# Kernel optimization log

Hardware: AMD Instinct MI355X
Metric: run time of the kernel (lower is better)

Reference implementation:

```python
import jax, jax.numpy as jnp
import numpy as np

N, E, D_IN, D, H, L, D_EMB, T = 4096, 131072, 72, 256, 8, 2, 128, 5
HD = D // H
LN_EPS = 1e-5


def _linear(x, w, b):
    # torch Linear: w is [out, in]
    return x @ w.T + b


def _layernorm(x, g, b):
    mu = jnp.mean(x, axis=-1, keepdims=True)
    var = jnp.var(x, axis=-1, keepdims=True)
    return (x - mu) * jax.lax.rsqrt(var + LN_EPS) * g + b


def _gps_layer(x, edge_index, p):
    src, dst = edge_index[0], edge_index[1]
    # GINConv: sum-aggregate neighbor messages, then MLP((1+eps)*x + agg)
    agg = jax.ops.segment_sum(x[src], dst, num_segments=N)
    h = (1.0 + p['gin_eps']) * x + agg
    h = _linear(jax.nn.elu(_linear(h, p['mlp_w1'], p['mlp_b1'])), p['mlp_w2'], p['mlp_b2'])
    h = jax.nn.elu(_layernorm(h, p['ln1_g'], p['ln1_b']))
    x = x + h

    # global multi-head self-attention over all N nodes (seq len = N)
    qkv = x @ p['attn_in_w'].T + p['attn_in_b']  # [N, 3D]
    q, k, v = jnp.split(qkv, 3, axis=-1)
    q = q.reshape(N, H, HD)
    k = k.reshape(N, H, HD)
    v = v.reshape(N, H, HD)
    scores = jnp.einsum('nhd,mhd->hnm', q, k) / np.sqrt(HD).astype(np.float32)
    attn = jax.nn.softmax(scores, axis=-1)
    o = jnp.einsum('hnm,mhd->nhd', attn, v).reshape(N, D)
    o = _linear(o, p['attn_out_w'], p['attn_out_b'])
    o = _layernorm(o, p['ln2_g'], p['ln2_b'])
    x = x + o

    # FFN (dim -> 2*dim -> dim, GELU)
    f = _linear(jax.nn.gelu(_linear(x, p['ffn_w1'], p['ffn_b1'])), p['ffn_w2'], p['ffn_b2'])
    f = _layernorm(f, p['ln3_g'], p['ln3_b'])
    return x + f


def setup_inputs() -> dict:
    key = jax.random.key(0)
    ks = iter(jax.random.split(key, 64))

    def w(shape, fan_in):
        return jax.random.normal(next(ks), shape, jnp.float32) * (1.0 / np.sqrt(fan_in))

    inp = {
        'x': jax.random.normal(next(ks), (N, D_IN), jnp.float32),
        'edge_index': jax.random.randint(next(ks), (2, E), 0, N, jnp.int64),
        'in_w': w((D, D_IN), D_IN), 'in_b': jnp.zeros((D,), jnp.float32),
        'head_w1': w((D_EMB, D), D), 'head_b1': jnp.zeros((D_EMB,), jnp.float32),
        'head_w2': w((T, D_EMB), D_EMB), 'head_b2': jnp.zeros((T,), jnp.float32),
    }
    # stacked per-layer params, leading axis L
    inp['mlp_w1'] = w((L, D, D), D); inp['mlp_b1'] = jnp.zeros((L, D), jnp.float32)
    inp['mlp_w2'] = w((L, D, D), D); inp['mlp_b2'] = jnp.zeros((L, D), jnp.float32)
    inp['gin_eps'] = jnp.zeros((L,), jnp.float32)
    inp['ln1_g'] = jnp.ones((L, D), jnp.float32); inp['ln1_b'] = jnp.zeros((L, D), jnp.float32)
    inp['attn_in_w'] = w((L, 3 * D, D), D); inp['attn_in_b'] = jnp.zeros((L, 3 * D), jnp.float32)
    inp['attn_out_w'] = w((L, D, D), D); inp['attn_out_b'] = jnp.zeros((L, D), jnp.float32)
    inp['ln2_g'] = jnp.ones((L, D), jnp.float32); inp['ln2_b'] = jnp.zeros((L, D), jnp.float32)
    inp['ffn_w1'] = w((L, 2 * D, D), D); inp['ffn_b1'] = jnp.zeros((L, 2 * D), jnp.float32)
    inp['ffn_w2'] = w((L, D, 2 * D), 2 * D); inp['ffn_b2'] = jnp.zeros((L, D), jnp.float32)
    inp['ln3_g'] = jnp.ones((L, D), jnp.float32); inp['ln3_b'] = jnp.zeros((L, D), jnp.float32)
    return inp


PER_LAYER = ['mlp_w1', 'mlp_b1', 'mlp_w2', 'mlp_b2', 'gin_eps', 'ln1_g', 'ln1_b',
             'attn_in_w', 'attn_in_b', 'attn_out_w', 'attn_out_b', 'ln2_g', 'ln2_b',
             'ffn_w1', 'ffn_b1', 'ffn_w2', 'ffn_b2', 'ln3_g', 'ln3_b']


def reference(x, edge_index, in_w, in_b, head_w1, head_b1, head_w2, head_b2,
              mlp_w1, mlp_b1, mlp_w2, mlp_b2, gin_eps, ln1_g, ln1_b,
              attn_in_w, attn_in_b, attn_out_w, attn_out_b, ln2_g, ln2_b,
              ffn_w1, ffn_b1, ffn_w2, ffn_b2, ln3_g, ln3_b):
    stacked = dict(mlp_w1=mlp_w1, mlp_b1=mlp_b1, mlp_w2=mlp_w2, mlp_b2=mlp_b2,
                   gin_eps=gin_eps, ln1_g=ln1_g, ln1_b=ln1_b,
                   attn_in_w=attn_in_w, attn_in_b=attn_in_b,
                   attn_out_w=attn_out_w, attn_out_b=attn_out_b,
                   ln2_g=ln2_g, ln2_b=ln2_b, ffn_w1=ffn_w1, ffn_b1=ffn_b1,
                   ffn_w2=ffn_w2, ffn_b2=ffn_b2, ln3_g=ln3_g, ln3_b=ln3_b)
    h = jax.nn.elu(_linear(x, in_w, in_b))  # input_proj (dropout/noise off in eval)
    for l in range(L):
        p = {k: v[l] for k, v in stacked.items()}
        h = _gps_layer(h, edge_index, p)
    out = _linear(jax.nn.elu(_linear(h, head_w1, head_b1)), head_w2, head_b2)
    return out
```

## Files before the change

### kernel.cpp

```cpp
#include <hip/hip_runtime.h>
#include <math.h>

#define NN 4096
#define NE 131072
#define DIM 256
#define NHEAD 8
#define HD 32

typedef __attribute__((ext_vector_type(8))) short short8v;
typedef __attribute__((ext_vector_type(4))) float f32x4;
#define MFMA16(a, b, c) __builtin_amdgcn_mfma_f32_16x16x32_bf16(a, b, c, 0, 0, 0)

__device__ __forceinline__ float elu_f(float v){ return v > 0.f ? v : expm1f(v); }
__device__ __forceinline__ float gelu_f(float v){
  const float c = 0.7978845608028654f;
  float t = tanhf(c * (v + 0.044715f * v * v * v));
  return 0.5f * v * (1.f + t);
}
__device__ __forceinline__ unsigned short f2bf(float f) {
  unsigned int u = __builtin_bit_cast(unsigned int, f);
  u += 0x7FFFu + ((u >> 16) & 1u);
  return (unsigned short)(u >> 16);
}
__device__ __forceinline__ unsigned int pk2(float a, float b) {
  return (unsigned int)f2bf(a) | ((unsigned int)f2bf(b) << 16);
}

__global__ void zero_counts(int* __restrict__ counts) {
  int i = blockIdx.x * 256 + threadIdx.x;
  if (i < NN) counts[i] = 0;
}

__global__ void count_edges(const int* __restrict__ ei, int* __restrict__ counts) {
  int e = blockIdx.x * 256 + threadIdx.x;
  if (e < NE) atomicAdd(&counts[ei[NE + e]], 1);
}

__global__ __launch_bounds__(1024) void scan_offsets(const int* __restrict__ counts,
                                                     int* __restrict__ offs,
                                                     int* __restrict__ cursor) {
  __shared__ int tmp[1024];
  int t = threadIdx.x;
  int base = t * 4;
  int c0 = counts[base], c1 = counts[base+1], c2 = counts[base+2], c3 = counts[base+3];
  int tsum = c0 + c1 + c2 + c3;
  tmp[t] = tsum;
  __syncthreads();
  for (int d = 1; d < 1024; d <<= 1) {
    int v = (t >= d) ? tmp[t - d] : 0;
    __syncthreads();
    tmp[t] += v;
    __syncthreads();
  }
  int excl = tmp[t] - tsum;
  offs[base]   = excl;           cursor[base]   = excl;
  offs[base+1] = excl + c0;      cursor[base+1] = excl + c0;
  offs[base+2] = excl + c0 + c1; cursor[base+2] = excl + c0 + c1;
  offs[base+3] = excl + c0 + c1 + c2; cursor[base+3] = excl + c0 + c1 + c2;
  if (t == 1023) offs[NN] = tmp[1023];
}

__global__ void scatter_edges(const int* __restrict__ ei, int* __restrict__ cursor,
                              int* __restrict__ esrc) {
  int e = blockIdx.x * 256 + threadIdx.x;
  if (e < NE) {
    int d = ei[NE + e];
    int pos = atomicAdd(&cursor[d], 1);
    esrc[pos] = ei[e];
  }
}

__global__ __launch_bounds__(256) void gin_agg(const int* __restrict__ offs,
                                               const int* __restrict__ esrc,
                                               const float* __restrict__ x,
                                               const float* __restrict__ eps_p, int l,
                                               unsigned short* __restrict__ aggb) {
  int n = blockIdx.x, c = threadIdx.x;
  int e0 = offs[n], e1 = offs[n + 1];
  float acc = 0.f;
  for (int e = e0; e < e1; e++) acc += x[(size_t)esrc[e] * DIM + c];
  float eps = eps_p[l];
  aggb[(size_t)n * DIM + c] = f2bf((1.f + eps) * x[(size_t)n * DIM + c] + acc);
}

template<int ACT, int WF32, int WBF16, int QSCALE>
__global__ __launch_bounds__(256) void gemm_mfma(
    const unsigned short* __restrict__ A, const unsigned short* __restrict__ W,
    const float* __restrict__ bias, float* __restrict__ Cf,
    unsigned short* __restrict__ Cb, int M, int N, int K)
{
  __shared__ __align__(16) unsigned short As[64][40];
  __shared__ __align__(16) unsigned short Ws[64][40];
  int t = threadIdx.x;
  int w = t >> 6, lane = t & 63, lo = lane & 15, g = lane >> 4;
  int wr = w >> 1, wc = w & 1;
  int bn = blockIdx.x * 64, bm = blockIdx.y * 64;
  int srow = t >> 2, skk = (t & 3) << 3;
  const unsigned short* ap = A + (size_t)(bm + srow) * K + skk;
  const unsigned short* wp = W + (size_t)(bn + srow) * K + skk;

  f32x4 acc[2][2] = {{{0.f,0.f,0.f,0.f},{0.f,0.f,0.f,0.f}},
                     {{0.f,0.f,0.f,0.f},{0.f,0.f,0.f,0.f}}};

  for (int k0 = 0; k0 < K; k0 += 32) {
    *(short8v*)&As[srow][skk] = *(const short8v*)(ap + k0);
    *(short8v*)&Ws[srow][skk] = *(const short8v*)(wp + k0);
    __syncthreads();
    short8v a0 = *(const short8v*)&As[wr * 32 + lo][8 * g];
    short8v a1 = *(const short8v*)&As[wr * 32 + 16 + lo][8 * g];
    short8v b0 = *(const short8v*)&Ws[wc * 32 + lo][8 * g];
    short8v b1 = *(const short8v*)&Ws[wc * 32 + 16 + lo][8 * g];
    acc[0][0] = MFMA16(a0, b0, acc[0][0]);
    acc[0][1] = MFMA16(a0, b1, acc[0][1]);
    acc[1][0] = MFMA16(a1, b0, acc[1][0]);
    acc[1][1] = MFMA16(a1, b1, acc[1][1]);
    __syncthreads();
  }

  #pragma unroll
  for (int mi = 0; mi < 2; mi++) {
    #pragma unroll
    for (int ni = 0; ni < 2; ni++) {
      #pragma unroll
      for (int r = 0; r < 4; r++) {
        int row = bm + wr * 32 + mi * 16 + 4 * g + r;
        int col = bn + wc * 32 + ni * 16 + lo;
        float v = acc[mi][ni][r] + bias[col];
        if (ACT == 1) v = elu_f(v);
        if (ACT == 2) v = gelu_f(v);
        if (QSCALE) { if (col < 256) v *= 0.17677669529663687f; }
        if (WF32) Cf[(size_t)row * N + col] = v;
        if (WBF16) Cb[(size_t)row * N + col] = f2bf(v);
      }
    }
  }
}

template<int ACT>
__global__ __launch_bounds__(256) void ln_act_add(const float* __restrict__ in,
                                                  const float* __restrict__ g,
                                                  const float* __restrict__ b,
                                                  float* __restrict__ x,
                                                  unsigned short* __restrict__ xb) {
  int rowb = blockIdx.x;
  int c = threadIdx.x;
  float v = in[(size_t)rowb * DIM + c];
  float s = v, s2 = v * v;
  #pragma unroll
  for (int off = 32; off >= 1; off >>= 1) {
    s  += __shfl_xor(s,  off, 64);
    s2 += __shfl_xor(s2, off, 64);
  }
  __shared__ float ws1[4], ws2[4];
  int w = threadIdx.x >> 6, lane = threadIdx.x & 63;
  if (lane == 0) { ws1[w] = s; ws2[w] = s2; }
  __syncthreads();
  s  = ws1[0] + ws1[1] + ws1[2] + ws1[3];
  s2 = ws2[0] + ws2[1] + ws2[2] + ws2[3];
  float mean = s * (1.f / DIM);
  float var = s2 * (1.f / DIM) - mean * mean;
  float r = rsqrtf(var + 1e-5f);
  float o = (v - mean) * r * g[c] + b[c];
  if (ACT == 1) o = elu_f(o);
  float nx = x[(size_t)rowb * DIM + c] + o;
  x[(size_t)rowb * DIM + c] = nx;
  xb[(size_t)rowb * DIM + c] = f2bf(nx);
}

__global__ __launch_bounds__(256) void vt_transpose(const unsigned short* __restrict__ tbb,
                                                    unsigned short* __restrict__ VT) {
  __shared__ unsigned short lds[128][33];
  int h = blockIdx.y;
  int nb = blockIdx.x * 128;
  int tid = threadIdx.x;
  int r8 = tid >> 5, d = tid & 31;
  #pragma unroll
  for (int i = 0; i < 16; i++) {
    int n = i * 8 + r8;
    lds[n][d] = tbb[(size_t)(nb + n) * 768 + 512 + h * 32 + d];
  }
  __syncthreads();
  int dd = tid >> 7, j = tid & 127;
  #pragma unroll
  for (int i = 0; i < 16; i++) {
    int d2 = i * 2 + dd;
    VT[((size_t)h * 32 + d2) * 4096 + nb + j] = lds[j][d2];
  }
}

__global__ __launch_bounds__(256) void attn_mfma_split(
    const unsigned short* __restrict__ qkvb, const unsigned short* __restrict__ VT,
    float* __restrict__ po, float* __restrict__ ml, int kspan) {
  __shared__ __align__(16) unsigned short Ks[2][64][40];
  __shared__ __align__(16) unsigned short Vs[2][32][72];
  int tid = threadIdx.x;
  int w = tid >> 6, lane = tid & 63;
  int lo = lane & 15, g = lane >> 4;
  int h = blockIdx.y;
  int s = blockIdx.z;
  int qb = blockIdx.x * 64 + w * 16;
  int k_lo = s * kspan, k_hi = k_lo + kspan;

  int krow = tid >> 2, kq = (tid & 3) * 8;
  int vrow = tid >> 3, vo = (tid & 7) * 8;
  const unsigned short* Kg = qkvb + 256 + h * 32;
  const unsigned short* Vg = VT + ((size_t)(h * 32 + vrow)) * 4096;

  short8v qf = *(const short8v*)(qkvb + (size_t)(qb + lo) * 768 + h * 32 + 8 * g);

  f32x4 acc0 = {0.f, 0.f, 0.f, 0.f};
  f32x4 acc1 = {0.f, 0.f, 0.f, 0.f};
  float m = -1e30f, l = 0.f;
  const f32x4 zf = {0.f, 0.f, 0.f, 0.f};

  {
    short8v rk0 = *(const short8v*)(Kg + (size_t)(k_lo + krow) * 768 + kq);
    short8v rv0 = *(const short8v*)(Vg + k_lo + vo);
    *(short8v*)&Ks[0][krow][kq] = rk0;
    *(short8v*)&Vs[0][vrow][vo] = rv0;
  }
  __syncthreads();

  int buf = 0;
  for (int kb = k_lo; kb < k_hi; kb += 64) {
    short8v rk, rv;
    bool more = (kb + 64 < k_hi);
    if (more) {
      rk = *(const short8v*)(Kg + (size_t)(kb + 64 + krow) * 768 + kq);
      rv = *(const short8v*)(Vg + kb + 64 + vo);
    }

    short8v kA0 = *(const short8v*)&Ks[buf][lo][8 * g];
    short8v kA1 = *(const short8v*)&Ks[buf][16 + lo][8 * g];
    short8v kA2 = *(const short8v*)&Ks[buf][32 + lo][8 * g];
    short8v kA3 = *(const short8v*)&Ks[buf][48 + lo][8 * g];
    f32x4 s0_ = MFMA16(kA0, qf, zf);
    f32x4 s1_ = MFMA16(kA1, qf, zf);
    f32x4 s2_ = MFMA16(kA2, qf, zf);
    f32x4 s3_ = MFMA16(kA3, qf, zf);

    float ta_ = fmaxf(fmaxf(fmaxf(s0_[0],s0_[1]), fmaxf(s0_[2],s0_[3])),
                      fmaxf(fmaxf(s1_[0],s1_[1]), fmaxf(s1_[2],s1_[3])));
    float tb_ = fmaxf(fmaxf(fmaxf(s2_[0],s2_[1]), fmaxf(s2_[2],s2_[3])),
                      fmaxf(fmaxf(s3_[0],s3_[1]), fmaxf(s3_[2],s3_[3])));
    float t_ = fmaxf(ta_, tb_);
    t_ = fmaxf(t_, __shfl_xor(t_, 16, 64));
    t_ = fmaxf(t_, __shfl_xor(t_, 32, 64));
    if (!__all(t_ <= m)) {
      float nm_ = fmaxf(m, t_);
      float f_ = __expf(m - nm_);
      m = nm_; l *= f_;
      acc0[0]*=f_; acc0[1]*=f_; acc0[2]*=f_; acc0[3]*=f_;
      acc1[0]*=f_; acc1[1]*=f_; acc1[2]*=f_; acc1[3]*=f_;
    }
    float p0_=__expf(s0_[0]-m), p1_=__expf(s0_[1]-m), p2_=__expf(s0_[2]-m), p3_=__expf(s0_[3]-m);
    float p4_=__expf(s1_[0]-m), p5_=__expf(s1_[1]-m), p6_=__expf(s1_[2]-m), p7_=__expf(s1_[3]-m);
    float p8_=__expf(s2_[0]-m), p9_=__expf(s2_[1]-m), pA_=__expf(s2_[2]-m), pB_=__expf(s2_[3]-m);
    float pC_=__expf(s3_[0]-m), pD_=__expf(s3_[1]-m), pE_=__expf(s3_[2]-m), pF_=__expf(s3_[3]-m);
    l += ((((p0_+p1_)+(p2_+p3_)) + ((p4_+p5_)+(p6_+p7_))) +
          (((p8_+p9_)+(pA_+pB_)) + ((pC_+pD_)+(pE_+pF_))));

    uint4 uA_ = { pk2(p0_,p1_), pk2(p2_,p3_), pk2(p4_,p5_), pk2(p6_,p7_) };
    uint4 uB_ = { pk2(p8_,p9_), pk2(pA_,pB_), pk2(pC_,pD_), pk2(pE_,pF_) };
    short8v pbA_ = __builtin_bit_cast(short8v, uA_);
    short8v pbB_ = __builtin_bit_cast(short8v, uB_);

    short4 Wa0 = *(const short4*)&Vs[buf][lo][4 * g];
    short4 Wa1 = *(const short4*)&Vs[buf][lo][16 + 4 * g];
    short4 Wa2 = *(const short4*)&Vs[buf][lo][32 + 4 * g];
    short4 Wa3 = *(const short4*)&Vs[buf][lo][48 + 4 * g];
    short4 Xa0 = *(const short4*)&Vs[buf][16 + lo][4 * g];
    short4 Xa1 = *(const short4*)&Vs[buf][16 + lo][16 + 4 * g];
    short4 Xa2 = *(const short4*)&Vs[buf][16 + lo][32 + 4 * g];
    short4 Xa3 = *(const short4*)&Vs[buf][16 + lo][48 + 4 * g];
    short8v va0_ = {Wa0.x,Wa0.y,Wa0.z,Wa0.w, Wa1.x,Wa1.y,Wa1.z,Wa1.w};
    short8v va1_ = {Wa2.x,Wa2.y,Wa2.z,Wa2.w, Wa3.x,Wa3.y,Wa3.z,Wa3.w};
    short8v vb0_ = {Xa0.x,Xa0.y,Xa0.z,Xa0.w, Xa1.x,Xa1.y,Xa1.z,Xa1.w};
    short8v vb1_ = {Xa2.x,Xa2.y,Xa2.z,Xa2.w, Xa3.x,Xa3.y,Xa3.z,Xa3.w};
    acc0 = MFMA16(va0_, pbA_, acc0);
    acc0 = MFMA16(va1_, pbB_, acc0);
    acc1 = MFMA16(vb0_, pbA_, acc1);
    acc1 = MFMA16(vb1_, pbB_, acc1);

    if (more) {
      *(short8v*)&Ks[buf ^ 1][krow][kq] = rk;
      *(short8v*)&Vs[buf ^ 1][vrow][vo] = rv;
    }
    __syncthreads();
    buf ^= 1;
  }

  l += __shfl_xor(l, 16, 64);
  l += __shfl_xor(l, 32, 64);

  int q = qb + lo;
  float* pr = po + ((size_t)s * NN + q) * DIM + h * 32 + 4 * g;
  *(f32x4*)pr = acc0;
  *(f32x4*)(pr + 16) = acc1;
  if (g == 0) {
    float2* mlp = (float2*)(ml + (((size_t)s * NN + q) * NHEAD + h) * 2);
    *mlp = float2{m, l};
  }
}

__global__ __launch_bounds__(256) void attn_merge(const float* __restrict__ po,
                                                  const float* __restrict__ ml,
                                                  unsigned short* __restrict__ attb, int S) {
  int q = blockIdx.x;
  int c = threadIdx.x;
  int h = c >> 5;
  float M = -1e30f;
  for (int s = 0; s < S; s++)
    M = fmaxf(M, ml[(((size_t)s * NN + q) * NHEAD + h) * 2]);
  float L = 0.f, O = 0.f;
  for (int s = 0; s < S; s++) {
    const float* mlp = ml + (((size_t)s * NN + q) * NHEAD + h) * 2;
    float e = __expf(mlp[0] - M);
    L += e * mlp[1];
    O += e * po[((size_t)s * NN + q) * DIM + c];
  }
  attb[(size_t)q * DIM + c] = f2bf(O / L);
}

#define WO0 0
#define WO1 131072
#define WO2 262144
#define WO3 655360
#define WO4 786432
#define WO5 1048576
#define WO6 1310720
#define WTOT 1343488
__global__ __launch_bounds__(256) void wconv(const float* __restrict__ s0, const float* __restrict__ s1,
                                             const float* __restrict__ s2, const float* __restrict__ s3,
                                             const float* __restrict__ s4, const float* __restrict__ s5,
                                             const float* __restrict__ s6, unsigned short* __restrict__ dst) {
  int i4 = (blockIdx.x * 256 + threadIdx.x) * 4;
  if (i4 >= WTOT) return;
  const float* src; int loc;
  if      (i4 < WO1) { src = s0; loc = i4 - WO0; }
  else if (i4 < WO2) { src = s1; loc = i4 - WO1; }
  else if (i4 < WO3) { src = s2; loc = i4 - WO2; }
  else if (i4 < WO4) { src = s3; loc = i4 - WO3; }
  else if (i4 < WO5) { src = s4; loc = i4 - WO4; }
  else if (i4 < WO6) { src = s5; loc = i4 - WO5; }
  else               { src = s6; loc = i4 - WO6; }
  float4 v = *(const float4*)(src + loc);
  ushort4 o;
  o.x = f2bf(v.x); o.y = f2bf(v.y); o.z = f2bf(v.z); o.w = f2bf(v.w);
  *(ushort4*)(dst + i4) = o;
}

__global__ __launch_bounds__(256) void pad72_96(const float* __restrict__ src,
                                                unsigned short* __restrict__ dst, int total) {
  int idx = blockIdx.x * 256 + threadIdx.x;
  if (idx >= total) return;
  int row = idx / 96, col = idx - row * 96;
  dst[idx] = (col < 72) ? f2bf(src[row * 72 + col]) : (unsigned short)0;
}

__global__ void head2_kernel(const float* __restrict__ e, const float* __restrict__ w,
                             const float* __restrict__ b, float* __restrict__ out) {
  int idx = blockIdx.x * 256 + threadIdx.x;
  if (idx >= NN * 5) return;
  int rowi = idx / 5, col = idx % 5;
  float s = b[col];
  const float* ep = e + (size_t)rowi * 128;
  const float* wp = w + (size_t)col * 128;
  #pragma unroll 16
  for (int k = 0; k < 128; k++) s += ep[k] * wp[k];
  out[idx] = s;
}

extern "C" void kernel_launch(void* const* d_in, const int* in_sizes, int n_in,
                              void* d_out, int out_size, void* d_ws, size_t ws_size,
                              hipStream_t stream) {
  const float* x_in   = (const float*)d_in[0];
  const int*   ei     = (const int*)  d_in[1];
  const float* in_w   = (const float*)d_in[2];
  const float* in_b   = (const float*)d_in[3];
  const float* head_w1= (const float*)d_in[4];
  const float* head_b1= (const float*)d_in[5];
  const float* head_w2= (const float*)d_in[6];
  const float* head_b2= (const float*)d_in[7];
  const float* mlp_w1 = (const float*)d_in[8];
  const float* mlp_b1 = (const float*)d_in[9];
  const float* mlp_w2 = (const float*)d_in[10];
  const float* mlp_b2 = (const float*)d_in[11];
  const float* gin_eps= (const float*)d_in[12];
  const float* ln1_g  = (const float*)d_in[13];
  const float* ln1_b  = (const float*)d_in[14];
  const float* attn_in_w = (const float*)d_in[15];
  const float* attn_in_b = (const float*)d_in[16];
  const float* attn_out_w= (const float*)d_in[17];
  const float* attn_out_b= (const float*)d_in[18];
  const float* ln2_g  = (const float*)d_in[19];
  const float* ln2_b  = (const float*)d_in[20];
  const float* ffn_w1 = (const float*)d_in[21];
  const float* ffn_b1 = (const float*)d_in[22];
  const float* ffn_w2 = (const float*)d_in[23];
  const float* ffn_b2 = (const float*)d_in[24];
  const float* ln3_g  = (const float*)d_in[25];
  const float* ln3_b  = (const float*)d_in[26];

  float* ws = (float*)d_ws;
  float* x    = ws;
  float* t2   = x  + (size_t)NN * DIM;
  float* he   = t2 + (size_t)NN * DIM;
  unsigned short* xb   = (unsigned short*)(he + (size_t)NN * 128);
  unsigned short* tbb  = xb   + (size_t)NN * DIM;
  unsigned short* aggb = tbb  + (size_t)NN * 768;
  unsigned short* attb = aggb + (size_t)NN * DIM;
  unsigned short* VT   = attb + (size_t)NN * DIM;
  unsigned short* xinb = VT   + (size_t)NN * DIM;
  unsigned short* inwb = xinb + (size_t)NN * 96;
  unsigned short* warena = inwb + 256 * 96;
  int* counts = (int*)(warena + WTOT);
  int* offs   = counts + NN;
  int* cursor = offs + NN + 1;
  int* esrc   = cursor + NN;
  float* po   = (float*)(esrc + NE);
  size_t used_f = (size_t)(po - ws);
  int S = 1;
  for (int cand = 4; cand >= 2; cand >>= 1) {
    size_t need = (used_f + (size_t)cand * NN * DIM + (size_t)cand * NN * NHEAD * 2) * 4;
    if (ws_size >= need) { S = cand; break; }
  }
  float* ml = po + (size_t)S * NN * DIM;
  int kspan = NN / S;

  const unsigned short* w_mlp1 = warena + WO0;
  const unsigned short* w_mlp2 = warena + WO1;
  const unsigned short* w_qkv  = warena + WO2;
  const unsigned short* w_aout = warena + WO3;
  const unsigned short* w_ffn1 = warena + WO4;
  const unsigned short* w_ffn2 = warena + WO5;
  const unsigned short* w_h1   = warena + WO6;

  zero_counts<<<16, 256, 0, stream>>>(counts);
  count_edges<<<NE / 256, 256, 0, stream>>>(ei, counts);
  scan_offsets<<<1, 1024, 0, stream>>>(counts, offs, cursor);
  scatter_edges<<<NE / 256, 256, 0, stream>>>(ei, cursor, esrc);

  wconv<<<1312, 256, 0, stream>>>(mlp_w1, mlp_w2, attn_in_w, attn_out_w, ffn_w1, ffn_w2,
                                  head_w1, warena);
  pad72_96<<<(NN * 96 + 255) / 256, 256, 0, stream>>>(x_in, xinb, NN * 96);
  pad72_96<<<(256 * 96 + 255) / 256, 256, 0, stream>>>(in_w, inwb, 256 * 96);

  gemm_mfma<1,1,1,0><<<dim3(DIM/64, NN/64), 256, 0, stream>>>(xinb, inwb, in_b, x, xb,
                                                              NN, DIM, 96);

  for (int l = 0; l < 2; l++) {
    gin_agg<<<NN, 256, 0, stream>>>(offs, esrc, x, gin_eps, l, aggb);
    gemm_mfma<1,0,1,0><<<dim3(4, 64), 256, 0, stream>>>(aggb, w_mlp1 + (size_t)l*65536,
                                                        mlp_b1 + l*DIM, nullptr, tbb,
                                                        NN, DIM, DIM);
    gemm_mfma<0,1,0,0><<<dim3(4, 64), 256, 0, stream>>>(tbb, w_mlp2 + (size_t)l*65536,
                                                        mlp_b2 + l*DIM, t2, nullptr,
                                                        NN, DIM, DIM);
    ln_act_add<1><<<NN, 256, 0, stream>>>(t2, ln1_g + l*DIM, ln1_b + l*DIM, x, xb);

    gemm_mfma<0,0,1,1><<<dim3(12, 64), 256, 0, stream>>>(xb, w_qkv + (size_t)l*196608,
                                                         attn_in_b + l*768, nullptr, tbb,
                                                         NN, 768, DIM);
    vt_transpose<<<dim3(32, 8), 256, 0, stream>>>(tbb, VT);
    attn_mfma_split<<<dim3(64, NHEAD, S), 256, 0, stream>>>(tbb, VT, po, ml, kspan);
    attn_merge<<<NN, 256, 0, stream>>>(po, ml, attb, S);
    gemm_mfma<0,1,0,0><<<dim3(4, 64), 256, 0, stream>>>(attb, w_aout + (size_t)l*65536,
                                                        attn_out_b + l*DIM, t2, nullptr,
                                                        NN, DIM, DIM);
    ln_act_add<0><<<NN, 256, 0, stream>>>(t2, ln2_g + l*DIM, ln2_b + l*DIM, x, xb);

    gemm_mfma<2,0,1,0><<<dim3(8, 64), 256, 0, stream>>>(xb, w_ffn1 + (size_t)l*131072,
                                                        ffn_b1 + l*512, nullptr, tbb,
                                                        NN, 512, DIM);
    gemm_mfma<0,1,0,0><<<dim3(4, 64), 256, 0, stream>>>(tbb, w_ffn2 + (size_t)l*131072,
                                                        ffn_b2 + l*DIM, t2, nullptr,
                                                        NN, DIM, 512);
    ln_act_add<0><<<NN, 256, 0, stream>>>(t2, ln3_g + l*DIM, ln3_b + l*DIM, x, xb);
  }

  gemm_mfma<1,1,0,0><<<dim3(2, 64), 256, 0, stream>>>(xb, w_h1, head_b1, he, nullptr,
                                                      NN, 128, DIM);
  head2_kernel<<<(NN * 5 + 255) / 256, 256, 0, stream>>>(he, head_w2, head_b2, (float*)d_out);
}
```

Baseline: 363.7 us.

## Use exp2 softmax, MFMA row sums, hardware bf16 pack, bf16 GIN gather

Folds log2(e) into the Q scaling so the attention softmax uses exp2 directly, and computes the running row sum with an extra MFMA against a ones vector instead of scalar adds and shuffles. Replaces the software bf16 rounding of probabilities with the v_cvt_pk_bf16_f32 instruction. The GIN aggregation now gathers neighbor features from the bf16 copy of x, halving gather traffic. The cost is extra MFMA work per tile and lower precision in the aggregation inputs.

After: 369.7 us. No clear change (+1.6%).

```diff
diff --git a/kernel.cpp b/kernel.cpp
--- a/kernel.cpp
+++ b/kernel.cpp
@@ -22,8 +22,13 @@
   u += 0x7FFFu + ((u >> 16) & 1u);
   return (unsigned short)(u >> 16);
 }
-__device__ __forceinline__ unsigned int pk2(float a, float b) {
-  return (unsigned int)f2bf(a) | ((unsigned int)f2bf(b) << 16);
+__device__ __forceinline__ float bf2f(unsigned short u) {
+  return __builtin_bit_cast(float, (unsigned int)u << 16);
+}
+__device__ __forceinline__ unsigned int cvtpk(float a, float b) {
+  unsigned int r;
+  asm("v_cvt_pk_bf16_f32 %0, %1, %2" : "=v"(r) : "v"(a), "v"(b));
+  return r;
 }
 
 __global__ void zero_counts(int* __restrict__ counts) {
@@ -72,15 +77,15 @@
 
 __global__ __launch_bounds__(256) void gin_agg(const int* __restrict__ offs,
                                                const int* __restrict__ esrc,
-                                               const float* __restrict__ x,
+                                               const unsigned short* __restrict__ xb,
                                                const float* __restrict__ eps_p, int l,
                                                unsigned short* __restrict__ aggb) {
   int n = blockIdx.x, c = threadIdx.x;
   int e0 = offs[n], e1 = offs[n + 1];
   float acc = 0.f;
-  for (int e = e0; e < e1; e++) acc += x[(size_t)esrc[e] * DIM + c];
+  for (int e = e0; e < e1; e++) acc += bf2f(xb[(size_t)esrc[e] * DIM + c]);
   float eps = eps_p[l];
-  aggb[(size_t)n * DIM + c] = f2bf((1.f + eps) * x[(size_t)n * DIM + c] + acc);
+  aggb[(size_t)n * DIM + c] = f2bf((1.f + eps) * bf2f(xb[(size_t)n * DIM + c]) + acc);
 }
 
 template<int ACT, int WF32, int WBF16, int QSCALE>
@@ -128,7 +133,7 @@
         float v = acc[mi][ni][r] + bias[col];
         if (ACT == 1) v = elu_f(v);
         if (ACT == 2) v = gelu_f(v);
-        if (QSCALE) { if (col < 256) v *= 0.17677669529663687f; }
+        if (QSCALE) { if (col < 256) v *= (0.17677669529663687f * 1.4426950408889634f); }
         if (WF32) Cf[(size_t)row * N + col] = v;
         if (WBF16) Cb[(size_t)row * N + col] = f2bf(v);
       }
@@ -210,8 +215,11 @@
 
   f32x4 acc0 = {0.f, 0.f, 0.f, 0.f};
   f32x4 acc1 = {0.f, 0.f, 0.f, 0.f};
-  float m = -1e30f, l = 0.f;
+  f32x4 accL = {0.f, 0.f, 0.f, 0.f};
+  float m = -1e30f;
   const f32x4 zf = {0.f, 0.f, 0.f, 0.f};
+  const short ONE = (short)0x3F80;
+  const short8v ones = {ONE, ONE, ONE, ONE, ONE, ONE, ONE, ONE};
 
   {
     short8v rk0 = *(const short8v*)(Kg + (size_t)(k_lo + krow) * 768 + kq);
@@ -248,20 +256,19 @@
     t_ = fmaxf(t_, __shfl_xor(t_, 32, 64));
     if (!__all(t_ <= m)) {
       float nm_ = fmaxf(m, t_);
-      float f_ = __expf(m - nm_);
-      m = nm_; l *= f_;
+      float f_ = exp2f(m - nm_);
+      m = nm_;
       acc0[0]*=f_; acc0[1]*=f_; acc0[2]*=f_; acc0[3]*=f_;
       acc1[0]*=f_; acc1[1]*=f_; acc1[2]*=f_; acc1[3]*=f_;
+      accL[0]*=f_; accL[1]*=f_; accL[2]*=f_; accL[3]*=f_;
     }
-    float p0_=__expf(s0_[0]-m), p1_=__expf(s0_[1]-m), p2_=__expf(s0_[2]-m), p3_=__expf(s0_[3]-m);
-    float p4_=__expf(s1_[0]-m), p5_=__expf(s1_[1]-m), p6_=__expf(s1_[2]-m), p7_=__expf(s1_[3]-m);
-    float p8_=__expf(s2_[0]-m), p9_=__expf(s2_[1]-m), pA_=__expf(s2_[2]-m), pB_=__expf(s2_[3]-m);
-    float pC_=__expf(s3_[0]-m), pD_=__expf(s3_[1]-m), pE_=__expf(s3_[2]-m), pF_=__expf(s3_[3]-m);
-    l += ((((p0_+p1_)+(p2_+p3_)) + ((p4_+p5_)+(p6_+p7_))) +
-          (((p8_+p9_)+(pA_+pB_)) + ((pC_+pD_)+(pE_+pF_))));
-
-    uint4 uA_ = { pk2(p0_,p1_), pk2(p2_,p3_), pk2(p4_,p5_), pk2(p6_,p7_) };
-    uint4 uB_ = { pk2(p8_,p9_), pk2(pA_,pB_), pk2(pC_,pD_), pk2(pE_,pF_) };
+    float p0_=exp2f(s0_[0]-m), p1_=exp2f(s0_[1]-m), p2_=exp2f(s0_[2]-m), p3_=exp2f(s0_[3]-m);
+    float p4_=exp2f(s1_[0]-m), p5_=exp2f(s1_[1]-m), p6_=exp2f(s1_[2]-m), p7_=exp2f(s1_[3]-m);
+    float p8_=exp2f(s2_[0]-m), p9_=exp2f(s2_[1]-m), pA_=exp2f(s2_[2]-m), pB_=exp2f(s2_[3]-m);
+    float pC_=exp2f(s3_[0]-m), pD_=exp2f(s3_[1]-m), pE_=exp2f(s3_[2]-m), pF_=exp2f(s3_[3]-m);
+
+    uint4 uA_ = { cvtpk(p0_,p1_), cvtpk(p2_,p3_), cvtpk(p4_,p5_), cvtpk(p6_,p7_) };
+    uint4 uB_ = { cvtpk(p8_,p9_), cvtpk(pA_,pB_), cvtpk(pC_,pD_), cvtpk(pE_,pF_) };
     short8v pbA_ = __builtin_bit_cast(short8v, uA_);
     short8v pbB_ = __builtin_bit_cast(short8v, uB_);
 
@@ -281,6 +288,8 @@
     acc0 = MFMA16(va1_, pbB_, acc0);
     acc1 = MFMA16(vb0_, pbA_, acc1);
     acc1 = MFMA16(vb1_, pbB_, acc1);
+    accL = MFMA16(ones, pbA_, accL);
+    accL = MFMA16(ones, pbB_, accL);
 
     if (more) {
       *(short8v*)&Ks[buf ^ 1][krow][kq] = rk;
@@ -290,16 +299,13 @@
     buf ^= 1;
   }
 
-  l += __shfl_xor(l, 16, 64);
-  l += __shfl_xor(l, 32, 64);
-
   int q = qb + lo;
   float* pr = po + ((size_t)s * NN + q) * DIM + h * 32 + 4 * g;
   *(f32x4*)pr = acc0;
   *(f32x4*)(pr + 16) = acc1;
   if (g == 0) {
     float2* mlp = (float2*)(ml + (((size_t)s * NN + q) * NHEAD + h) * 2);
-    *mlp = float2{m, l};
+    *mlp = float2{m, accL[0]};
   }
 }
 
@@ -315,7 +321,7 @@
   float L = 0.f, O = 0.f;
   for (int s = 0; s < S; s++) {
     const float* mlp = ml + (((size_t)s * NN + q) * NHEAD + h) * 2;
-    float e = __expf(mlp[0] - M);
+    float e = exp2f(mlp[0] - M);
     L += e * mlp[1];
     O += e * po[((size_t)s * NN + q) * DIM + c];
   }
@@ -450,7 +456,7 @@
                                                               NN, DIM, 96);
 
   for (int l = 0; l < 2; l++) {
-    gin_agg<<<NN, 256, 0, stream>>>(offs, esrc, x, gin_eps, l, aggb);
+    gin_agg<<<NN, 256, 0, stream>>>(offs, esrc, xb, gin_eps, l, aggb);
     gemm_mfma<1,0,1,0><<<dim3(4, 64), 256, 0, stream>>>(aggb, w_mlp1 + (size_t)l*65536,
                                                         mlp_b1 + l*DIM, nullptr, tbb,
                                                         NN, DIM, DIM);
```
